# Kernel tuning notes

Measured on AMD Instinct MI355X. Metric: run time of the kernel, lower is better.

Reference implementation:

```python
import jax, jax.numpy as jnp
import numpy as np
from jax import lax

NUM_SAMPLE_POINTS = 1024
BIG = jnp.float32(1e10)  # stands in for +inf, fp16-safe


def setup_inputs() -> dict:
    key = jax.random.key(0)
    input = jax.random.normal(key, (8, 65536, 3), dtype=jnp.float32)
    return {"input": input}


def _fps_indices(points, num_samples):
    # points: [B, N, 3] -> indices [B, num_samples] int32
    B, N, _ = points.shape

    def step(carry, _):
        min_dist, farthest = carry  # [B, N], [B]
        cur = jnp.take_along_axis(points, farthest[:, None, None], axis=1)  # [B,1,3]
        d = jnp.sum((points - cur) ** 2, axis=-1)  # [B, N] squared distances
        min_dist = jnp.minimum(min_dist, d)
        nxt = jnp.argmax(min_dist, axis=-1).astype(jnp.int32)  # [B]
        return (min_dist, nxt), farthest

    init = (jnp.full((B, N), BIG, dtype=points.dtype), jnp.zeros((B,), jnp.int32))
    _, idx = lax.scan(step, init, None, length=num_samples)  # idx: [M, B]
    return idx.T  # [B, M]


def reference(input):
    # Faithful FPS: iteratively pick the point farthest from the selected set,
    # starting from index 0 (standard PointNet++ convention).
    idx = _fps_indices(input, NUM_SAMPLE_POINTS)  # [B, M] int32
    sampled = jnp.take_along_axis(input, idx[:, :, None], axis=1)  # [B, M, 3]
    return idx, sampled
```

## Files before the change

kernel.cpp:

```cpp
#include <hip/hip_runtime.h>


#define NB    8
#define NPTS  65536
#define NSAMP 1024
#define WPB   32
#define TPB   512
#define NWAVE 8
#define PPT   4
#define RECQ  16

typedef unsigned long long ull;

#define DPP(x, ctrl) \
  ((unsigned)__builtin_amdgcn_update_dpp((int)(x), (int)(x), (ctrl), 0xf, 0xf, false))

__device__ __forceinline__ unsigned umax_wave64(unsigned x) {
  unsigned t;
  t = DPP(x, 0x111); x = t > x ? t : x;
  t = DPP(x, 0x112); x = t > x ? t : x;
  t = DPP(x, 0x114); x = t > x ? t : x;
  t = DPP(x, 0x118); x = t > x ? t : x;
  t = DPP(x, 0x142); x = t > x ? t : x;
  t = DPP(x, 0x143); x = t > x ? t : x;
  return (unsigned)__builtin_amdgcn_readlane((int)x, 63);
}
__device__ __forceinline__ unsigned umax_low8(unsigned x) {
  unsigned t;
  t = DPP(x, 0x111); x = t > x ? t : x;
  t = DPP(x, 0x112); x = t > x ? t : x;
  t = DPP(x, 0x114); x = t > x ? t : x;
  return (unsigned)__builtin_amdgcn_readlane((int)x, 7);
}

__device__ __forceinline__ void ld3_issue(const ull* p, ull& a, ull& b, ull& c) {
  asm volatile(
      "global_load_dwordx2 %0, %3, off sc0\n\t"
      "global_load_dwordx2 %1, %3, off offset:8 sc0\n\t"
      "global_load_dwordx2 %2, %3, off offset:16 sc0"
      : "=&v"(a), "=&v"(b), "=&v"(c) : "v"(p) : "memory");
}
__device__ __forceinline__ void wait3_touch(ull& a, ull& b, ull& c) {
  asm volatile("s_waitcnt vmcnt(3)" : "+v"(a), "+v"(b), "+v"(c) :: "memory");
}
__device__ __forceinline__ void wait_vm0() {
  asm volatile("s_waitcnt vmcnt(0)" ::: "memory");
}
__device__ __forceinline__ void st3_sc0(ull* p, ull a, ull b, ull c) {
  asm volatile(
      "global_store_dwordx2 %3, %0, off sc0\n\t"
      "global_store_dwordx2 %3, %1, off offset:8 sc0\n\t"
      "global_store_dwordx2 %3, %2, off offset:16 sc0"
      :: "v"(a), "v"(b), "v"(c), "v"(p) : "memory");
}

__device__ __forceinline__ void stage2_pack(const unsigned (*red)[5], int lane,
                                            ull tag, ull& w0, ull& w1, ull& w2,
                                            int& ewin) {
  const int e = lane & 7;
  const unsigned d2 = red[e][0];
  const unsigned nn = red[e][1];
  const unsigned mx = umax_low8(d2);
  const ull bb = __ballot(d2 == mx) & 0xFFull;
  if (__popcll(bb) == 1) {
    ewin = __ffsll(bb) - 1;
  } else {
    const unsigned v = (d2 == mx) ? (65535u - nn) : 0u;
    const unsigned mv = umax_low8(v);
    const ull b2 = __ballot((d2 == mx) && (v == mv)) & 0xFFull;
    ewin = __ffsll(b2) - 1;
  }
  const ull k2 = ((ull)d2 << 16) | (ull)(65535u - nn);
  const unsigned xb = red[e][2], yb = red[e][3], zb = red[e][4];
  w0 = (k2 << 16) | tag;
  w1 = ((ull)xb << 32) | ((ull)(yb >> 16) << 16) | tag;
  w2 = ((ull)(yb & 0xFFFFu) << 48) | ((ull)zb << 16) | tag;
}

__global__ __launch_bounds__(TPB, 4)
void fps_kernel(const float* __restrict__ pts, float* __restrict__ out,
                ull* __restrict__ ws) {
  const int wg   = blockIdx.x;
  const int b    = wg >> 5;
  const int w    = wg & 31;
  const int tid  = threadIdx.x;
  const int lane = tid & 63;
  const int wave = tid >> 6;

  const float* p = pts + (size_t)b * NPTS * 3;

  float px[PPT], py[PPT], pz[PPT], md[PPT];
#pragma unroll
  for (int i = 0; i < PPT; ++i) {
    const int n = w * (TPB * PPT) + i * TPB + tid;
    px[i] = p[3 * n + 0];
    py[i] = p[3 * n + 1];
    pz[i] = p[3 * n + 2];
    md[i] = 1e10f;
  }

  float cx = p[0], cy = p[1], cz = p[2];

  ull* baseL = ws + (size_t)b * (2 * WPB * RECQ);
  ull* baseI = ws + (size_t)NB * (2 * WPB * RECQ) + (size_t)b * (2 * WPB * RECQ);

  float* out_idx = out + (size_t)b * NSAMP;
  float* out_smp = out + (size_t)NB * NSAMP + (size_t)b * NSAMP * 3;

  if (w == 0 && tid == 0) {
    out_idx[0] = 0.0f;
    out_smp[0] = cx; out_smp[1] = cy; out_smp[2] = cz;
  }

  __shared__ unsigned red[NWAVE][5];
  __shared__ float4 bc4;
  __shared__ int bn2;

  bool useIF = false;

  for (int t = 0; t < NSAMP - 1; ++t) {
    float bv = -1.0f; int bi = 0;
#pragma unroll
    for (int i = 0; i < PPT; ++i) {
      const float dx = __fsub_rn(px[i], cx);
      const float dy = __fsub_rn(py[i], cy);
      const float dz = __fsub_rn(pz[i], cz);
      const float d  = __fadd_rn(__fadd_rn(__fmul_rn(dx, dx), __fmul_rn(dy, dy)),
                                 __fmul_rn(dz, dz));
      const float m = fminf(md[i], d);
      md[i] = m;
      if (m > bv) { bv = m; bi = i; }
    }

    const unsigned dbits = __float_as_uint(bv);
    const unsigned mw = umax_wave64(dbits);
    const bool tied = (dbits == mw);
    const ull bal0 = __ballot(tied);
    int wlane;
    if (__popcll(bal0) == 1) {
      wlane = __ffsll(bal0) - 1;
    } else {
      ull sel = 0;
#pragma unroll
      for (int ii = 0; ii < PPT; ++ii) {
        const ull bb = __ballot(tied && (bi == ii));
        const bool take = (sel == 0) && (bb != 0);
        sel = take ? bb : sel;
      }
      wlane = __ffsll(sel) - 1;
    }
    if (lane == wlane) {
      const bool c1 = (bi & 1), c2 = (bi & 2);
      const float qx = c2 ? (c1 ? px[3] : px[2]) : (c1 ? px[1] : px[0]);
      const float qy = c2 ? (c1 ? py[3] : py[2]) : (c1 ? py[1] : py[0]);
      const float qz = c2 ? (c1 ? pz[3] : pz[2]) : (c1 ? pz[1] : pz[0]);
      red[wave][0] = dbits;
      red[wave][1] = (unsigned)(w * (TPB * PPT) + bi * TPB + tid);
      red[wave][2] = __float_as_uint(qx);
      red[wave][3] = __float_as_uint(qy);
      red[wave][4] = __float_as_uint(qz);
    }
    __syncthreads();

    const ull tag = (ull)(unsigned)(t + 1);
    const int par = t & 1;

    if (wave == 1) {
      ull w0, w1, w2; int ewin;
      stage2_pack(red, lane, tag, w0, w1, w2, ewin);
      if (lane == ewin) {
        st3_sc0(baseL + (size_t)(par * WPB + w) * RECQ, w0, w1, w2);
        ull* recI = baseI + (size_t)(par * WPB + w) * RECQ;
        __hip_atomic_store(recI + 0, w0, __ATOMIC_RELAXED, __HIP_MEMORY_SCOPE_AGENT);
        __hip_atomic_store(recI + 1, w1, __ATOMIC_RELAXED, __HIP_MEMORY_SCOPE_AGENT);
        __hip_atomic_store(recI + 2, w2, __ATOMIC_RELAXED, __HIP_MEMORY_SCOPE_AGENT);
      }
    } else if (wave == 0) {
      const size_t roff = (size_t)(par * WPB + (lane & 31)) * RECQ;
      const ull* recL = baseL + roff;
      const ull* recI = baseI + roff;
      const bool mine = (lane < WPB);
      ull r0 = 0, r1 = 0, r2 = 0;
      bool s = !mine;

      if (!useIF) {
        if (mine) {
          ull a0, a1, a2, b0, b1, b2;
          bool fromA = true, hit = false;
          ld3_issue(recL, a0, a1, a2);
          for (int it = 0; it < 128; ++it) {
            ld3_issue(recL, b0, b1, b2);
            wait3_touch(a0, a1, a2);
            bool m = ((a0 & 0xFFFFull) == tag) & ((a1 & 0xFFFFull) == tag) &
                     ((a2 & 0xFFFFull) == tag);
            if (__all(m)) { hit = true; fromA = true; break; }
            ld3_issue(recL, a0, a1, a2);
            wait3_touch(b0, b1, b2);
            m = ((b0 & 0xFFFFull) == tag) & ((b1 & 0xFFFFull) == tag) &
                ((b2 & 0xFFFFull) == tag);
            if (__all(m)) { hit = true; fromA = false; break; }
          }
          wait_vm0();
          if (hit) {
            if (fromA) { r0 = a0; r1 = a1; r2 = a2; }
            else       { r0 = b0; r1 = b1; r2 = b2; }
            s = true;
          }
        }
      }

      if (!__all(s)) {
        useIF = true;
        bool done = !mine;
        for (;;) {
          if (!done) {
            r0 = __hip_atomic_load(recI + 0, __ATOMIC_RELAXED, __HIP_MEMORY_SCOPE_AGENT);
            r1 = __hip_atomic_load(recI + 1, __ATOMIC_RELAXED, __HIP_MEMORY_SCOPE_AGENT);
            r2 = __hip_atomic_load(recI + 2, __ATOMIC_RELAXED, __HIP_MEMORY_SCOPE_AGENT);
            done = ((r0 & 0xFFFFull) == tag) & ((r1 & 0xFFFFull) == tag) &
                   ((r2 & 0xFFFFull) == tag);
          }
          if (__all(done)) break;
          __builtin_amdgcn_s_sleep(1);
        }
      }

      const unsigned d3  = (unsigned)(r0 >> 32);
      const unsigned lnv = (unsigned)((r0 >> 16) & 0xFFFFull);
      const unsigned m3 = umax_wave64(d3);
      const ull b3 = __ballot(d3 == m3);
      int src;
      if (__popcll(b3) == 1) {
        src = __ffsll(b3) - 1;
      } else {
        const unsigned v = (d3 == m3) ? lnv : 0u;
        const unsigned mv = umax_wave64(v);
        const ull b4 = __ballot((d3 == m3) && (v == mv));
        src = __ffsll(b4) - 1;
      }
      const float xx = __uint_as_float((unsigned)(r1 >> 32));
      const float yy = __uint_as_float(((unsigned)((r1 >> 16) & 0xFFFFull) << 16) |
                                       (unsigned)(r2 >> 48));
      const float zz = __uint_as_float((unsigned)((r2 >> 16) & 0xFFFFFFFFull));
      const int n2   = 65535 - (int)__shfl((int)lnv, src, 64);
      const float wx = __shfl(xx, src, 64);
      const float wy = __shfl(yy, src, 64);
      const float wz = __shfl(zz, src, 64);
      if (lane == 0) {
        bc4 = make_float4(wx, wy, wz, 0.0f);
        bn2 = n2;
      }
    }
    __syncthreads();

    const float4 c4 = bc4;
    if (w == 0 && wave == 2 && lane == 0) {
      out_idx[t + 1] = (float)bn2;
      out_smp[(t + 1) * 3 + 0] = c4.x;
      out_smp[(t + 1) * 3 + 1] = c4.y;
      out_smp[(t + 1) * 3 + 2] = c4.z;
    }
    cx = c4.x; cy = c4.y; cz = c4.z;
  }
}

extern "C" void kernel_launch(void* const* d_in, const int* in_sizes, int n_in,
                              void* d_out, int out_size, void* d_ws, size_t ws_size,
                              hipStream_t stream) {
  (void)in_sizes; (void)n_in; (void)out_size; (void)ws_size;
  const float* pts = (const float*)d_in[0];
  float* out = (float*)d_out;
  ull* ws = (ull*)d_ws;
  fps_kernel<<<dim3(NB * WPB), dim3(TPB), 0, stream>>>(pts, out, ws);
}
```

Baseline: 2.141 ms.

## Replace intra-block barrier and wave reduction with LDS atomic max and last-arriver publish

Removes the first __syncthreads per iteration and the separate wave-1 stage-2 reduction over per-wave records. Each wave's winning lane instead does an LDS 64-bit atomic fetch_max on a packed key (distance, inverted index, wave id), and a counter identifies the last-arriving wave, which publishes the block's record to global memory. Wave 0 then polls as before. This shortens the critical path per FPS step, but it relies on the atomic ordering in LDS for correctness, relies on the parity-indexed key cell being reset, and adds atomic contention.

```diff
diff --git a/kernel.cpp b/kernel.cpp
--- a/kernel.cpp
+++ b/kernel.cpp
@@ -25,13 +25,6 @@
   t = DPP(x, 0x143); x = t > x ? t : x;
   return (unsigned)__builtin_amdgcn_readlane((int)x, 63);
 }
-__device__ __forceinline__ unsigned umax_low8(unsigned x) {
-  unsigned t;
-  t = DPP(x, 0x111); x = t > x ? t : x;
-  t = DPP(x, 0x112); x = t > x ? t : x;
-  t = DPP(x, 0x114); x = t > x ? t : x;
-  return (unsigned)__builtin_amdgcn_readlane((int)x, 7);
-}
 
 __device__ __forceinline__ void ld3_issue(const ull* p, ull& a, ull& b, ull& c) {
   asm volatile(
@@ -52,29 +45,6 @@
       "global_store_dwordx2 %3, %1, off offset:8 sc0\n\t"
       "global_store_dwordx2 %3, %2, off offset:16 sc0"
       :: "v"(a), "v"(b), "v"(c), "v"(p) : "memory");
-}
-
-__device__ __forceinline__ void stage2_pack(const unsigned (*red)[5], int lane,
-                                            ull tag, ull& w0, ull& w1, ull& w2,
-                                            int& ewin) {
-  const int e = lane & 7;
-  const unsigned d2 = red[e][0];
-  const unsigned nn = red[e][1];
-  const unsigned mx = umax_low8(d2);
-  const ull bb = __ballot(d2 == mx) & 0xFFull;
-  if (__popcll(bb) == 1) {
-    ewin = __ffsll(bb) - 1;
-  } else {
-    const unsigned v = (d2 == mx) ? (65535u - nn) : 0u;
-    const unsigned mv = umax_low8(v);
-    const ull b2 = __ballot((d2 == mx) && (v == mv)) & 0xFFull;
-    ewin = __ffsll(b2) - 1;
-  }
-  const ull k2 = ((ull)d2 << 16) | (ull)(65535u - nn);
-  const unsigned xb = red[e][2], yb = red[e][3], zb = red[e][4];
-  w0 = (k2 << 16) | tag;
-  w1 = ((ull)xb << 32) | ((ull)(yb >> 16) << 16) | tag;
-  w2 = ((ull)(yb & 0xFFFFu) << 48) | ((ull)zb << 16) | tag;
 }
 
 __global__ __launch_bounds__(TPB, 4)
@@ -112,9 +82,14 @@
     out_smp[0] = cx; out_smp[1] = cy; out_smp[2] = cz;
   }
 
-  __shared__ unsigned red[NWAVE][5];
+  __shared__ unsigned red[NWAVE][4];
+  __shared__ ull keyCell[2];
+  __shared__ unsigned cnt;
   __shared__ float4 bc4;
   __shared__ int bn2;
+
+  if (tid == 0) { keyCell[0] = 0; keyCell[1] = 0; cnt = 0; }
+  __syncthreads();
 
   bool useIF = false;
 
@@ -149,33 +124,48 @@
       }
       wlane = __ffsll(sel) - 1;
     }
+
+    const ull tag = (ull)(unsigned)(t + 1);
+    const int par = t & 1;
+
     if (lane == wlane) {
       const bool c1 = (bi & 1), c2 = (bi & 2);
       const float qx = c2 ? (c1 ? px[3] : px[2]) : (c1 ? px[1] : px[0]);
       const float qy = c2 ? (c1 ? py[3] : py[2]) : (c1 ? py[1] : py[0]);
       const float qz = c2 ? (c1 ? pz[3] : pz[2]) : (c1 ? pz[1] : pz[0]);
-      red[wave][0] = dbits;
-      red[wave][1] = (unsigned)(w * (TPB * PPT) + bi * TPB + tid);
-      red[wave][2] = __float_as_uint(qx);
-      red[wave][3] = __float_as_uint(qy);
-      red[wave][4] = __float_as_uint(qz);
-    }
-    __syncthreads();
-
-    const ull tag = (ull)(unsigned)(t + 1);
-    const int par = t & 1;
-
-    if (wave == 1) {
-      ull w0, w1, w2; int ewin;
-      stage2_pack(red, lane, tag, w0, w1, w2, ewin);
-      if (lane == ewin) {
-        st3_sc0(baseL + (size_t)(par * WPB + w) * RECQ, w0, w1, w2);
-        ull* recI = baseI + (size_t)(par * WPB + w) * RECQ;
-        __hip_atomic_store(recI + 0, w0, __ATOMIC_RELAXED, __HIP_MEMORY_SCOPE_AGENT);
-        __hip_atomic_store(recI + 1, w1, __ATOMIC_RELAXED, __HIP_MEMORY_SCOPE_AGENT);
-        __hip_atomic_store(recI + 2, w2, __ATOMIC_RELAXED, __HIP_MEMORY_SCOPE_AGENT);
-      }
-    } else if (wave == 0) {
+      red[wave][0] = __float_as_uint(qx);
+      red[wave][1] = __float_as_uint(qy);
+      red[wave][2] = __float_as_uint(qz);
+      const unsigned n = (unsigned)(w * (TPB * PPT) + bi * TPB + tid);
+      const ull key = ((ull)dbits << 32) | ((ull)(65535u - n) << 16) |
+                      ((ull)(unsigned)wave << 8);
+      __hip_atomic_fetch_max(&keyCell[par], key, __ATOMIC_RELEASE,
+                             __HIP_MEMORY_SCOPE_WORKGROUP);
+    }
+    unsigned ret = 0;
+    if (lane == 0)
+      ret = __hip_atomic_fetch_add(&cnt, 1u, __ATOMIC_ACQ_REL,
+                                   __HIP_MEMORY_SCOPE_WORKGROUP);
+    const int isLast = __shfl((int)(ret == 8u * (unsigned)t + 7u), 0, 64);
+
+    if (isLast && lane == 0) {
+      const ull kk = __hip_atomic_load(&keyCell[par], __ATOMIC_ACQUIRE,
+                                       __HIP_MEMORY_SCOPE_WORKGROUP);
+      const int e = (int)((kk >> 8) & 7ull);
+      const unsigned xb = red[e][0], yb = red[e][1], zb = red[e][2];
+      const ull w0 = (kk & 0xFFFFFFFFFFFF0000ull) | tag;
+      const ull w1 = ((ull)xb << 32) | ((ull)(yb >> 16) << 16) | tag;
+      const ull w2 = ((ull)(yb & 0xFFFFu) << 48) | ((ull)zb << 16) | tag;
+      const size_t slot = (size_t)(par * WPB + w) * RECQ;
+      st3_sc0(baseL + slot, w0, w1, w2);
+      ull* recI = baseI + slot;
+      __hip_atomic_store(recI + 0, w0, __ATOMIC_RELAXED, __HIP_MEMORY_SCOPE_AGENT);
+      __hip_atomic_store(recI + 1, w1, __ATOMIC_RELAXED, __HIP_MEMORY_SCOPE_AGENT);
+      __hip_atomic_store(recI + 2, w2, __ATOMIC_RELAXED, __HIP_MEMORY_SCOPE_AGENT);
+    }
+
+    if (wave == 0) {
+      wait_vm0();
       const size_t roff = (size_t)(par * WPB + (lane & 31)) * RECQ;
       const ull* recL = baseL + roff;
       const ull* recI = baseI + roff;
@@ -254,11 +244,14 @@
     __syncthreads();
 
     const float4 c4 = bc4;
-    if (w == 0 && wave == 2 && lane == 0) {
-      out_idx[t + 1] = (float)bn2;
-      out_smp[(t + 1) * 3 + 0] = c4.x;
-      out_smp[(t + 1) * 3 + 1] = c4.y;
-      out_smp[(t + 1) * 3 + 2] = c4.z;
+    if (wave == 2 && lane == 0) {
+      keyCell[par] = 0;
+      if (w == 0) {
+        out_idx[t + 1] = (float)bn2;
+        out_smp[(t + 1) * 3 + 0] = c4.x;
+        out_smp[(t + 1) * 3 + 1] = c4.y;
+        out_smp[(t + 1) * 3 + 2] = c4.z;
+      }
     }
     cx = c4.x; cy = c4.y; cz = c4.z;
   }
```

Result: slower. 2.286 ms (+6.8%).
